# Performance work log

Hardware: AMD Instinct MI355X
Metric: run time of the kernel (lower is better)

The kernel has to match this reference:

```python
import jax, jax.numpy as jnp
import numpy as np

BSZ, SL, D, K, KU, KY, NPAD = 2, 1024, 768, 16, 3, 2, 2048


def setup_inputs() -> dict:
    key = jax.random.key(0)
    ks = jax.random.split(key, 8)
    s = 1.0 / np.sqrt(D).astype(np.float32)
    return {
        "inputs": jax.random.normal(ks[0], (BSZ, SL, D), dtype=jnp.float32),
        "sigma": jax.random.uniform(ks[1], (K,), dtype=jnp.float32, minval=1e-3, maxval=1.0),
        "V": jax.random.normal(ks[2], (SL, K), dtype=jnp.float32),
        "M_u": jax.random.normal(ks[3], (KU, D, D), dtype=jnp.float32) * s,
        "M_phi_plus": jax.random.normal(ks[4], (K, D, D), dtype=jnp.float32) * s,
        "M_phi_minus": jax.random.normal(ks[5], (K, D, D), dtype=jnp.float32) * s,
        "M_y": jax.random.normal(ks[6], (D, KY, D), dtype=jnp.float32) * s,
        "padded_sl": NPAD,
    }


def _shift(x, i):
    # prepend i zeros along the time axis, drop the last i steps
    if i == 0:
        return x
    return jnp.pad(x, ((0, 0), (i, 0), (0, 0)))[:, : x.shape[1]]


def _forward(inputs, sigma, V, M_u, M_phi_plus, M_phi_minus, M_y, padded_sl,
             use_ar_u=True, use_ar_y=True):
    bsz, sl, d = inputs.shape
    n = padded_sl
    sgn = jnp.where(jnp.arange(sl) % 2 == 0, 1.0, -1.0).astype(inputs.dtype)[None, :, None]
    # --- FFT long convolution of inputs against K spectral filters (compute_spectral) ---
    v_f = jnp.fft.rfft(V, n=n, axis=0)                           # (nf, K)
    u_k = jnp.stack([inputs, inputs * sgn], axis=-1)             # (b, sl, d, 2): plus / alternating-sign branches
    U_f = jnp.fft.rfft(u_k, n=n, axis=1)                         # (b, nf, d, 2)
    prod = v_f[None, :, :, None, None] * U_f[:, :, None, :, :]   # (b, nf, K, d, 2)
    U_conv = jnp.fft.irfft(prod, n=n, axis=1)[:, :sl]            # (b, sl, K, d, 2)
    U_plus = U_conv[..., 0]
    U_minus = U_conv[..., 1] * sgn[..., None]
    scale = sigma ** 0.25                                        # (K,) Hankel eigenvalue scaling
    spectral = (jnp.einsum('blkd,k,kdo->blo', U_plus, scale, M_phi_plus)
                + jnp.einsum('blkd,k,kdo->blo', U_minus, scale, M_phi_minus))
    if use_ar_y:
        spectral = _shift(spectral, 2)
    y_t = spectral
    if use_ar_u:
        # compute_ar_u: sum_i M_u[i] @ u_{t-i}
        ar_u = sum(jnp.einsum('bld,do->blo', _shift(inputs, i), M_u[i])
                   for i in range(M_u.shape[0]))
        y_t = y_t + ar_u
    if use_ar_y:
        # compute_ar_y: sum_{i=1..k_y} M_y[:, i-1, :] @ y_{t-i}
        ar_y = sum(jnp.einsum('bld,od->blo', _shift(y_t, i + 1), M_y[:, i, :])
                   for i in range(M_y.shape[1]))
        y_t = y_t + ar_y
    return y_t


def reference(inputs, sigma, V, M_u, M_phi_plus, M_phi_minus, M_y, padded_sl):
    # dropout rate is 0.0 -> identity at both dropout sites
    return _forward(inputs, sigma, V, M_u, M_phi_plus, M_phi_minus, M_y, padded_sl)
```

## Files before the change

### kernel.cpp

```cpp
#include <hip/hip_runtime.h>
#include <cstddef>
#include <cstdint>

#define SLEN 1024
#define DIM  768
#define NJ   32
#define KSPEC (NJ * DIM)
#define KTOT  (KSPEC + 3 * DIM)
#define MROWS (2 * SLEN)
#define SK1 8
#define SK2 4

typedef _Float16 f16;
typedef _Float16 f16x8 __attribute__((ext_vector_type(8)));
typedef _Float16 f16x4 __attribute__((ext_vector_type(4)));
typedef float    f32x4 __attribute__((ext_vector_type(4)));

__device__ __forceinline__ void async16(f16* lds, const f16* g) {
    __builtin_amdgcn_global_load_lds(
        (const __attribute__((address_space(1))) unsigned int*)g,
        (__attribute__((address_space(3))) unsigned int*)lds, 16, 0, 0);
}

__global__ __launch_bounds__(256) void build_r8(
    const float* __restrict__ sigma, const float* __restrict__ V,
    f16* __restrict__ R8, float* __restrict__ zb)
{
    int g = blockIdx.x * 256 + threadIdx.x;
    if (g < 256) zb[g] = 0.f;
    int j = g / 1536, i = g % 1536;
    int k = j & 15;
    int tau = 1031 - i;
    float val = 0.f;
    if (tau >= 0 && tau < 1024) {
        val = powf(sigma[k], 0.25f) * V[tau * 16 + k];
        if (j >= 16 && (tau & 1)) val = -val;
    }
    R8[j * 1536 + i] = (f16)val;
}

__global__ __launch_bounds__(256) void pack_x(
    const float* __restrict__ x, f16* __restrict__ x16, f16* __restrict__ x16t)
{
    __shared__ float tile[32][33];
    const int b  = blockIdx.z;
    const int d0 = blockIdx.y * 32;
    const int t0 = blockIdx.x * 32;
    const int tx = threadIdx.x & 31, ty = threadIdx.x >> 5;
#pragma unroll
    for (int r = 0; r < 4; ++r) {
        int tl = ty + r * 8;
        float v = x[(size_t)(b * SLEN + t0 + tl) * DIM + d0 + tx];
        tile[tl][tx] = v;
        x16[(size_t)(b * SLEN + t0 + tl) * DIM + d0 + tx] = (f16)v;
    }
    __syncthreads();
#pragma unroll
    for (int r = 0; r < 4; ++r) {
        int dl = ty + r * 8;
        x16t[((size_t)b * DIM + d0 + dl) * SLEN + t0 + tx] = (f16)tile[tx][dl];
    }
}

__global__ __launch_bounds__(256) void pack_w(
    const float* __restrict__ Mpp, const float* __restrict__ Mpm,
    const float* __restrict__ Mu, f16* __restrict__ W16t)
{
    __shared__ float tile[32][33];
    const int c0 = blockIdx.x * 32;
    const int o0 = blockIdx.y * 32;
    const int tx = threadIdx.x & 31, ty = threadIdx.x >> 5;
#pragma unroll
    for (int r = 0; r < 4; ++r) {
        int cl = ty + r * 8;
        int c = c0 + cl;
        const float* src;
        if (c < 12288)      src = Mpp + (size_t)c * DIM;
        else if (c < KSPEC) src = Mpm + (size_t)(c - 12288) * DIM;
        else                src = Mu  + (size_t)(c - KSPEC) * DIM;
        tile[cl][tx] = src[o0 + tx];
    }
    __syncthreads();
#pragma unroll
    for (int r = 0; r < 4; ++r) {
        int ol = ty + r * 8;
        W16t[(size_t)(o0 + ol) * KTOT + c0 + tx] = (f16)tile[tx][ol];
    }
}

__global__ __launch_bounds__(256) void pack_my(
    const float* __restrict__ My, f16* __restrict__ My16t)
{
    int g = blockIdx.x * 256 + threadIdx.x;
    float4 v = ((const float4*)My)[g];
    f16x4 h = {(f16)v.x, (f16)v.y, (f16)v.z, (f16)v.w};
    ((f16x4*)My16t)[g] = h;
}

__global__ __launch_bounds__(256) void conv_mfma(
    const f16* __restrict__ xt, const f16* __restrict__ R8,
    f16* __restrict__ U16)
{
    __shared__ f16 Bs[128 * 64];
    __shared__ f16 Cp[8 * 264];
    const int d0 = blockIdx.x * 128;
    const int l0 = blockIdx.y * 128;
    const int b  = blockIdx.z >> 5;
    const int j  = blockIdx.z & 31;
    const int tid = threadIdx.x;
    const int lane = tid & 63, w = tid >> 6;
    const int wr = w >> 1, wc = w & 1;
    const int lrow = lane & 15, lgrp = lane >> 4;
    const int rrel = lane >> 3, slotw = lane & 7;
    const int colh = (slotw ^ rrel) * 8;

    f32x4 acc[4][4];
#pragma unroll
    for (int mi = 0; mi < 4; ++mi)
#pragma unroll
        for (int ni = 0; ni < 4; ++ni) acc[mi][ni] = (f32x4){0.f, 0.f, 0.f, 0.f};

    const f16* R8j = R8 + j * 1536;
    const f16* xb  = xt + ((size_t)b * DIM + d0) * SLEN;
    const int cch = tid / 33;
    const int cjc = (tid % 33) * 8;
    const int nkt = (l0 >> 6) + 2;

    for (int kt = 0; kt < nkt; ++kt) {
        const int t0 = kt * 64;
        const int base = 904 - l0 + t0;
        {
            const f16* gp = R8j + base + cjc - cch;
            f16x8 v;
#pragma unroll
            for (int e = 0; e < 8; ++e) v[e] = gp[e];
            *(f16x8*)&Cp[cch * 264 + cjc] = v;
            if (tid < 8) {
                int ch2 = tid + 256;
                int c2 = ch2 / 33, jc2 = (ch2 % 33) * 8;
                const f16* gp2 = R8j + base + jc2 - c2;
                f16x8 v2;
#pragma unroll
                for (int e = 0; e < 8; ++e) v2[e] = gp2[e];
                *(f16x8*)&Cp[c2 * 264 + jc2] = v2;
            }
        }
#pragma unroll
        for (int q = 0; q < 4; ++q) {
            int row = w * 32 + q * 8 + rrel;
            async16(&Bs[(w * 32 + q * 8) * 64],
                    xb + (size_t)row * SLEN + t0 + colh);
        }
        __syncthreads();
#pragma unroll
        for (int ks = 0; ks < 2; ++ks) {
            f16x8 af[4], bf[4];
#pragma unroll
            for (int mi = 0; mi < 4; ++mi) {
                int r = wr * 64 + mi * 16 + lrow;
                int h = 127 - r + ks * 32 + lgrp * 8;
                int c = (-h) & 7;
                af[mi] = *(const f16x8*)&Cp[c * 265 + h];
            }
#pragma unroll
            for (int ni = 0; ni < 4; ++ni) {
                int col = wc * 64 + ni * 16 + lrow;
                int slot = (ks * 4 + lgrp) ^ (col & 7);
                bf[ni] = *(const f16x8*)&Bs[col * 64 + slot * 8];
            }
#pragma unroll
            for (int mi = 0; mi < 4; ++mi)
#pragma unroll
                for (int ni = 0; ni < 4; ++ni)
                    acc[mi][ni] = __builtin_amdgcn_mfma_f32_16x16x32_f16(
                        af[mi], bf[ni], acc[mi][ni], 0, 0, 0);
        }
        __syncthreads();
    }
    const size_t ub = (size_t)b * SLEN * KSPEC + (size_t)j * DIM;
#pragma unroll
    for (int mi = 0; mi < 4; ++mi)
#pragma unroll
        for (int ni = 0; ni < 4; ++ni) {
            int l = l0 + wr * 64 + mi * 16 + lgrp * 4;
            int d = d0 + wc * 64 + ni * 16 + lrow;
#pragma unroll
            for (int q = 0; q < 4; ++q)
                U16[ub + (size_t)(l + q) * KSPEC + d] = (f16)acc[mi][ni][q];
        }
}

__global__ __launch_bounds__(256) void gemm1_mfma(
    const f16* __restrict__ U16, const f16* __restrict__ x16,
    const f16* __restrict__ W16t, const f16* __restrict__ zb16,
    float* __restrict__ P)
{
    __shared__ f16 As[128 * 64];
    __shared__ f16 Bs[128 * 64];
    const int n0 = blockIdx.x * 128;
    const int m0 = blockIdx.y * 128;
    const int s  = blockIdx.z;
    const int tid = threadIdx.x;
    const int lane = tid & 63, w = tid >> 6;
    const int wr = w >> 1, wc = w & 1;
    const int lrow = lane & 15, lgrp = lane >> 4;
    const int rrel = lane >> 3, slotw = lane & 7;
    const int colh = (slotw ^ rrel) * 8;

    f32x4 acc[4][4];
#pragma unroll
    for (int mi = 0; mi < 4; ++mi)
#pragma unroll
        for (int ni = 0; ni < 4; ++ni) acc[mi][ni] = (f32x4){0.f, 0.f, 0.f, 0.f};

    const int kts = (420 * s) >> 3, kte = (420 * (s + 1)) >> 3;
    for (int kt = kts; kt < kte; ++kt) {
        const int c0 = kt * 64;
#pragma unroll
        for (int q = 0; q < 4; ++q) {
            int row = w * 32 + q * 8 + rrel;
            int m = m0 + row;
            int l = m & (SLEN - 1);
            const f16* src;
            if (c0 < KSPEC) {
                src = (l >= 2) ? U16 + (size_t)(m - 2) * KSPEC + c0 + colh : zb16;
            } else {
                int cr = c0 - KSPEC;
                int i  = cr / DIM;
                src = (l >= i) ? x16 + (size_t)(m - i) * DIM + (cr - i * DIM) + colh
                               : zb16;
            }
            async16(&As[(w * 32 + q * 8) * 64], src);
        }
#pragma unroll
        for (int q = 0; q < 4; ++q) {
            int row = w * 32 + q * 8 + rrel;
            async16(&Bs[(w * 32 + q * 8) * 64],
                    W16t + (size_t)(n0 + row) * KTOT + c0 + colh);
        }
        __syncthreads();
#pragma unroll
        for (int ks = 0; ks < 2; ++ks) {
            f16x8 af[4], bf[4];
#pragma unroll
            for (int mi = 0; mi < 4; ++mi) {
                int r = wr * 64 + mi * 16 + lrow;
                int slot = (ks * 4 + lgrp) ^ (r & 7);
                af[mi] = *(const f16x8*)&As[r * 64 + slot * 8];
            }
#pragma unroll
            for (int ni = 0; ni < 4; ++ni) {
                int col = wc * 64 + ni * 16 + lrow;
                int slot = (ks * 4 + lgrp) ^ (col & 7);
                bf[ni] = *(const f16x8*)&Bs[col * 64 + slot * 8];
            }
#pragma unroll
            for (int mi = 0; mi < 4; ++mi)
#pragma unroll
                for (int ni = 0; ni < 4; ++ni)
                    acc[mi][ni] = __builtin_amdgcn_mfma_f32_16x16x32_f16(
                        af[mi], bf[ni], acc[mi][ni], 0, 0, 0);
        }
        __syncthreads();
    }
    float* Pp = P + (size_t)s * MROWS * DIM;
#pragma unroll
    for (int mi = 0; mi < 4; ++mi)
#pragma unroll
        for (int ni = 0; ni < 4; ++ni) {
            int m = m0 + wr * 64 + mi * 16 + lgrp * 4;
            int col = n0 + wc * 64 + ni * 16 + lrow;
#pragma unroll
            for (int q = 0; q < 4; ++q)
                Pp[(size_t)(m + q) * DIM + col] = acc[mi][ni][q];
        }
}

__global__ __launch_bounds__(256) void reduce8(
    const float* __restrict__ P, float* __restrict__ z, f16* __restrict__ z16)
{
    int g = blockIdx.x * 256 + threadIdx.x;
    const float4* P4 = (const float4*)P;
    float4 s = P4[g];
#pragma unroll
    for (int i = 1; i < SK1; ++i) {
        float4 t = P4[g + (size_t)i * 393216];
        s.x += t.x; s.y += t.y; s.z += t.z; s.w += t.w;
    }
    ((float4*)z)[g] = s;
    f16x4 h = {(f16)s.x, (f16)s.y, (f16)s.z, (f16)s.w};
    ((f16x4*)z16)[g] = h;
}

__global__ __launch_bounds__(256) void gemm2_mfma(
    const f16* __restrict__ z16, const f16* __restrict__ My16t,
    const f16* __restrict__ zb16, float* __restrict__ P2)
{
    __shared__ f16 As[128 * 64];
    __shared__ f16 Bs[128 * 64];
    const int n0 = blockIdx.x * 128;
    const int m0 = blockIdx.y * 128;
    const int s  = blockIdx.z;
    const int tid = threadIdx.x;
    const int lane = tid & 63, w = tid >> 6;
    const int wr = w >> 1, wc = w & 1;
    const int lrow = lane & 15, lgrp = lane >> 4;
    const int rrel = lane >> 3, slotw = lane & 7;
    const int colh = (slotw ^ rrel) * 8;

    f32x4 acc[4][4];
#pragma unroll
    for (int mi = 0; mi < 4; ++mi)
#pragma unroll
        for (int ni = 0; ni < 4; ++ni) acc[mi][ni] = (f32x4){0.f, 0.f, 0.f, 0.f};

    for (int kt = s * 6; kt < (s + 1) * 6; ++kt) {
        const int c0 = kt * 64;
        const int i = (c0 >= DIM) ? 1 : 0;
        const int sh = i + 1;
        const int co = c0 - i * DIM;
#pragma unroll
        for (int q = 0; q < 4; ++q) {
            int row = w * 32 + q * 8 + rrel;
            int m = m0 + row;
            int l = m & (SLEN - 1);
            const f16* src = (l >= sh)
                ? z16 + (size_t)(m - sh) * DIM + co + colh : zb16;
            async16(&As[(w * 32 + q * 8) * 64], src);
        }
#pragma unroll
        for (int q = 0; q < 4; ++q) {
            int row = w * 32 + q * 8 + rrel;
            async16(&Bs[(w * 32 + q * 8) * 64],
                    My16t + (size_t)(n0 + row) * 1536 + c0 + colh);
        }
        __syncthreads();
#pragma unroll
        for (int ks = 0; ks < 2; ++ks) {
            f16x8 af[4], bf[4];
#pragma unroll
            for (int mi = 0; mi < 4; ++mi) {
                int r = wr * 64 + mi * 16 + lrow;
                int slot = (ks * 4 + lgrp) ^ (r & 7);
                af[mi] = *(const f16x8*)&As[r * 64 + slot * 8];
            }
#pragma unroll
            for (int ni = 0; ni < 4; ++ni) {
                int col = wc * 64 + ni * 16 + lrow;
                int slot = (ks * 4 + lgrp) ^ (col & 7);
                bf[ni] = *(const f16x8*)&Bs[col * 64 + slot * 8];
            }
#pragma unroll
            for (int mi = 0; mi < 4; ++mi)
#pragma unroll
                for (int ni = 0; ni < 4; ++ni)
                    acc[mi][ni] = __builtin_amdgcn_mfma_f32_16x16x32_f16(
                        af[mi], bf[ni], acc[mi][ni], 0, 0, 0);
        }
        __syncthreads();
    }
    float* Pp = P2 + (size_t)s * MROWS * DIM;
#pragma unroll
    for (int mi = 0; mi < 4; ++mi)
#pragma unroll
        for (int ni = 0; ni < 4; ++ni) {
            int m = m0 + wr * 64 + mi * 16 + lgrp * 4;
            int col = n0 + wc * 64 + ni * 16 + lrow;
#pragma unroll
            for (int q = 0; q < 4; ++q)
                Pp[(size_t)(m + q) * DIM + col] = acc[mi][ni][q];
        }
}

__global__ __launch_bounds__(256) void final_add(
    const float* __restrict__ z, const float* __restrict__ P2,
    float* __restrict__ out)
{
    int g = blockIdx.x * 256 + threadIdx.x;
    const float4* z4 = (const float4*)z;
    const float4* Q  = (const float4*)P2;
    float4 s = z4[g];
#pragma unroll
    for (int i = 0; i < SK2; ++i) {
        float4 t = Q[g + (size_t)i * 393216];
        s.x += t.x; s.y += t.y; s.z += t.z; s.w += t.w;
    }
    ((float4*)out)[g] = s;
}

extern "C" void kernel_launch(void* const* d_in, const int* in_sizes, int n_in,
                              void* d_out, int out_size, void* d_ws, size_t ws_size,
                              hipStream_t stream)
{
    const float* inputs = (const float*)d_in[0];
    const float* sigma  = (const float*)d_in[1];
    const float* V      = (const float*)d_in[2];
    const float* Mu     = (const float*)d_in[3];
    const float* Mpp    = (const float*)d_in[4];
    const float* Mpm    = (const float*)d_in[5];
    const float* My     = (const float*)d_in[6];
    float* out = (float*)d_out;

    char* base = (char*)d_ws;
    float* zb   = (float*)(base);
    f16* R8     = (f16*)(base + 1024);
    f16* x16    = (f16*)(base + 99328);
    f16* x16t   = (f16*)(base + 3245056);
    f16* W16t   = (f16*)(base + 6390784);
    f16* My16t  = (f16*)(base + 47678464);
    f16* U16    = (f16*)(base + 50037760);
    f16* z16    = (f16*)(base + 150701056);
    float* P    = (float*)(base + 153846784);
    float* z    = (float*)(base + 204178432);
    const f16* zb16 = (const f16*)zb;

    build_r8<<<192, 256, 0, stream>>>(sigma, V, R8, zb);
    pack_x<<<dim3(32, 24, 2), 256, 0, stream>>>(inputs, x16, x16t);
    pack_w<<<dim3(840, 24), 256, 0, stream>>>(Mpp, Mpm, Mu, W16t);
    pack_my<<<1152, 256, 0, stream>>>(My, My16t);
    conv_mfma<<<dim3(6, 8, 64), 256, 0, stream>>>(x16t, R8, U16);
    gemm1_mfma<<<dim3(6, 16, SK1), 256, 0, stream>>>(U16, x16, W16t, zb16, P);
    reduce8<<<1536, 256, 0, stream>>>(P, z, z16);
    gemm2_mfma<<<dim3(6, 16, SK2), 256, 0, stream>>>(z16, My16t, zb16, P);
    final_add<<<1536, 256, 0, stream>>>(z, P, out);
}
```

Baseline: 390.7 us.

## Reorder spectral path: project inputs by filter weights first, then convolve in time

The code now applies the M_phi projection (with the sigma^0.25 scale folded into the weights) to the inputs first, through one large GEMM. It then runs the Toeplitz time convolution on the projected outputs and accumulates over filters inside conv_b. Before, it convolved the inputs for all 32 filter branches and then ran a K=24576 GEMM. The AR-u term is split into its own GEMM and the split-K reduction is adjusted to match. The aim is to avoid writing and re-reading the large convolved intermediate and to lower the total FLOPs. In exchange, the intermediate Yt (32×768 by 2048 rows) must still be written and read, and the fp16 rounding happens at a different point.

Result: slower. 483.0 us (+23.6%).

```diff
diff --git a/kernel.cpp b/kernel.cpp
--- a/kernel.cpp
+++ b/kernel.cpp
@@ -5,11 +5,11 @@
 #define SLEN 1024
 #define DIM  768
 #define NJ   32
-#define KSPEC (NJ * DIM)
-#define KTOT  (KSPEC + 3 * DIM)
+#define NSPEC (NJ * DIM)
 #define MROWS (2 * SLEN)
-#define SK1 8
-#define SK2 4
+#define NP    (MROWS * DIM)
+#define SKAR  2
+#define SK2   4
 
 typedef _Float16 f16;
 typedef _Float16 f16x8 __attribute__((ext_vector_type(8)));
@@ -23,8 +23,7 @@
 }
 
 __global__ __launch_bounds__(256) void build_r8(
-    const float* __restrict__ sigma, const float* __restrict__ V,
-    f16* __restrict__ R8, float* __restrict__ zb)
+    const float* __restrict__ V, f16* __restrict__ R8, float* __restrict__ zb)
 {
     int g = blockIdx.x * 256 + threadIdx.x;
     if (g < 256) zb[g] = 0.f;
@@ -33,58 +32,61 @@
     int tau = 1031 - i;
     float val = 0.f;
     if (tau >= 0 && tau < 1024) {
-        val = powf(sigma[k], 0.25f) * V[tau * 16 + k];
+        val = V[tau * 16 + k];
         if (j >= 16 && (tau & 1)) val = -val;
     }
     R8[j * 1536 + i] = (f16)val;
 }
 
-__global__ __launch_bounds__(256) void pack_x(
-    const float* __restrict__ x, f16* __restrict__ x16, f16* __restrict__ x16t)
+__global__ __launch_bounds__(256) void pack_x16(
+    const float* __restrict__ x, f16* __restrict__ x16)
+{
+    int g = blockIdx.x * 256 + threadIdx.x;
+    float4 v = ((const float4*)x)[g];
+    f16x4 h = {(f16)v.x, (f16)v.y, (f16)v.z, (f16)v.w};
+    ((f16x4*)x16)[g] = h;
+}
+
+__global__ __launch_bounds__(256) void pack_wA(
+    const float* __restrict__ Mpp, const float* __restrict__ Mpm,
+    const float* __restrict__ sigma, f16* __restrict__ WAt)
 {
     __shared__ float tile[32][33];
-    const int b  = blockIdx.z;
-    const int d0 = blockIdx.y * 32;
-    const int t0 = blockIdx.x * 32;
+    const int d0 = blockIdx.x * 32, o0 = blockIdx.y * 32, j = blockIdx.z;
+    const int k = j & 15;
+    const float* src = (j < 16 ? Mpp : Mpm) + (size_t)k * DIM * DIM;
+    const float sc = powf(sigma[k], 0.25f);
     const int tx = threadIdx.x & 31, ty = threadIdx.x >> 5;
-#pragma unroll
-    for (int r = 0; r < 4; ++r) {
-        int tl = ty + r * 8;
-        float v = x[(size_t)(b * SLEN + t0 + tl) * DIM + d0 + tx];
-        tile[tl][tx] = v;
-        x16[(size_t)(b * SLEN + t0 + tl) * DIM + d0 + tx] = (f16)v;
-    }
-    __syncthreads();
 #pragma unroll
     for (int r = 0; r < 4; ++r) {
         int dl = ty + r * 8;
-        x16t[((size_t)b * DIM + d0 + dl) * SLEN + t0 + tx] = (f16)tile[tx][dl];
-    }
-}
-
-__global__ __launch_bounds__(256) void pack_w(
-    const float* __restrict__ Mpp, const float* __restrict__ Mpm,
-    const float* __restrict__ Mu, f16* __restrict__ W16t)
-{
-    __shared__ float tile[32][33];
-    const int c0 = blockIdx.x * 32;
-    const int o0 = blockIdx.y * 32;
-    const int tx = threadIdx.x & 31, ty = threadIdx.x >> 5;
-#pragma unroll
-    for (int r = 0; r < 4; ++r) {
-        int cl = ty + r * 8;
-        int c = c0 + cl;
-        const float* src;
-        if (c < 12288)      src = Mpp + (size_t)c * DIM;
-        else if (c < KSPEC) src = Mpm + (size_t)(c - 12288) * DIM;
-        else                src = Mu  + (size_t)(c - KSPEC) * DIM;
-        tile[cl][tx] = src[o0 + tx];
+        tile[dl][tx] = src[(size_t)(d0 + dl) * DIM + o0 + tx];
     }
     __syncthreads();
 #pragma unroll
     for (int r = 0; r < 4; ++r) {
         int ol = ty + r * 8;
-        W16t[(size_t)(o0 + ol) * KTOT + c0 + tx] = (f16)tile[tx][ol];
+        WAt[(size_t)(j * DIM + o0 + ol) * DIM + d0 + tx] = (f16)(sc * tile[tx][ol]);
+    }
+}
+
+__global__ __launch_bounds__(256) void pack_mu(
+    const float* __restrict__ Mu, f16* __restrict__ Mut)
+{
+    __shared__ float tile[32][33];
+    const int d0 = blockIdx.x * 32, o0 = blockIdx.y * 32, i = blockIdx.z;
+    const float* src = Mu + (size_t)i * DIM * DIM;
+    const int tx = threadIdx.x & 31, ty = threadIdx.x >> 5;
+#pragma unroll
+    for (int r = 0; r < 4; ++r) {
+        int dl = ty + r * 8;
+        tile[dl][tx] = src[(size_t)(d0 + dl) * DIM + o0 + tx];
+    }
+    __syncthreads();
+#pragma unroll
+    for (int r = 0; r < 4; ++r) {
+        int ol = ty + r * 8;
+        Mut[(size_t)(o0 + ol) * 2304 + i * DIM + d0 + tx] = (f16)tile[tx][ol];
     }
 }
 
@@ -97,16 +99,15 @@
     ((f16x4*)My16t)[g] = h;
 }
 
-__global__ __launch_bounds__(256) void conv_mfma(
-    const f16* __restrict__ xt, const f16* __restrict__ R8,
-    f16* __restrict__ U16)
-{
-    __shared__ f16 Bs[128 * 64];
-    __shared__ f16 Cp[8 * 264];
-    const int d0 = blockIdx.x * 128;
-    const int l0 = blockIdx.y * 128;
-    const int b  = blockIdx.z >> 5;
-    const int j  = blockIdx.z & 31;
+__global__ __launch_bounds__(256) void gemmA(
+    const f16* __restrict__ x16, const f16* __restrict__ WAt,
+    f16* __restrict__ Yt)
+{
+    __shared__ f16 smem[128 * 132];
+    f16* As = smem;
+    f16* Bs = smem + 8192;
+    const int n0 = blockIdx.x * 128;
+    const int m0 = blockIdx.y * 128;
     const int tid = threadIdx.x;
     const int lane = tid & 63, w = tid >> 6;
     const int wr = w >> 1, wc = w & 1;
@@ -120,36 +121,16 @@
 #pragma unroll
         for (int ni = 0; ni < 4; ++ni) acc[mi][ni] = (f32x4){0.f, 0.f, 0.f, 0.f};
 
-    const f16* R8j = R8 + j * 1536;
-    const f16* xb  = xt + ((size_t)b * DIM + d0) * SLEN;
-    const int cch = tid / 33;
-    const int cjc = (tid % 33) * 8;
-    const int nkt = (l0 >> 6) + 2;
-
-    for (int kt = 0; kt < nkt; ++kt) {
-        const int t0 = kt * 64;
-        const int base = 904 - l0 + t0;
-        {
-            const f16* gp = R8j + base + cjc - cch;
-            f16x8 v;
-#pragma unroll
-            for (int e = 0; e < 8; ++e) v[e] = gp[e];
-            *(f16x8*)&Cp[cch * 264 + cjc] = v;
-            if (tid < 8) {
-                int ch2 = tid + 256;
-                int c2 = ch2 / 33, jc2 = (ch2 % 33) * 8;
-                const f16* gp2 = R8j + base + jc2 - c2;
-                f16x8 v2;
-#pragma unroll
-                for (int e = 0; e < 8; ++e) v2[e] = gp2[e];
-                *(f16x8*)&Cp[c2 * 264 + jc2] = v2;
-            }
-        }
+#pragma unroll 1
+    for (int kt = 0; kt < 12; ++kt) {
+        const int c0 = kt * 64;
 #pragma unroll
         for (int q = 0; q < 4; ++q) {
             int row = w * 32 + q * 8 + rrel;
+            async16(&As[(w * 32 + q * 8) * 64],
+                    x16 + (size_t)(m0 + row) * DIM + c0 + colh);
             async16(&Bs[(w * 32 + q * 8) * 64],
-                    xb + (size_t)row * SLEN + t0 + colh);
+                    WAt + (size_t)(n0 + row) * DIM + c0 + colh);
         }
         __syncthreads();
 #pragma unroll
@@ -158,9 +139,8 @@
 #pragma unroll
             for (int mi = 0; mi < 4; ++mi) {
                 int r = wr * 64 + mi * 16 + lrow;
-                int h = 127 - r + ks * 32 + lgrp * 8;
-                int c = (-h) & 7;
-                af[mi] = *(const f16x8*)&Cp[c * 265 + h];
+                int slot = (ks * 4 + lgrp) ^ (r & 7);
+                af[mi] = *(const f16x8*)&As[r * 64 + slot * 8];
             }
 #pragma unroll
             for (int ni = 0; ni < 4; ++ni) {
@@ -177,23 +157,127 @@
         }
         __syncthreads();
     }
-    const size_t ub = (size_t)b * SLEN * KSPEC + (size_t)j * DIM;
 #pragma unroll
     for (int mi = 0; mi < 4; ++mi)
 #pragma unroll
         for (int ni = 0; ni < 4; ++ni) {
-            int l = l0 + wr * 64 + mi * 16 + lgrp * 4;
-            int d = d0 + wc * 64 + ni * 16 + lrow;
+            int col = wc * 64 + ni * 16 + lrow;
+            int rowm = wr * 64 + mi * 16 + lgrp * 4;
+            f16x4 hv = {(f16)acc[mi][ni][0], (f16)acc[mi][ni][1],
+                        (f16)acc[mi][ni][2], (f16)acc[mi][ni][3]};
+            *(f16x4*)&smem[col * 132 + rowm] = hv;
+        }
+    __syncthreads();
+    {
+        int row = tid >> 1, half = tid & 1;
+        const f16* cr = &smem[row * 132 + half * 64];
+        f16* gp = Yt + (size_t)(n0 + row) * MROWS + m0 + half * 64;
+#pragma unroll
+        for (int e = 0; e < 16; ++e)
+            *(f16x4*)&gp[e * 4] = *(const f16x4*)&cr[e * 4];
+    }
+}
+
+__global__ __launch_bounds__(256) void conv_b(
+    const f16* __restrict__ Yt, const f16* __restrict__ R8,
+    float* __restrict__ P)
+{
+    __shared__ f16 Bs[128 * 64];
+    __shared__ f16 Cp[8 * 264];
+    const int o0 = blockIdx.x * 128;
+    const int meff = blockIdx.y ^ 7;
+    const int b = meff >> 3, yp = meff & 7;
+    const int l0 = yp * 128, m0 = meff * 128;
+    const int jg = blockIdx.z;
+    const int tid = threadIdx.x;
+    const int lane = tid & 63, w = tid >> 6;
+    const int wr = w >> 1, wc = w & 1;
+    const int lrow = lane & 15, lgrp = lane >> 4;
+    const int rrel = lane >> 3, slotw = lane & 7;
+    const int colh = (slotw ^ rrel) * 8;
+    const int cch = tid / 33, cjc = (tid % 33) * 8;
+
+    f32x4 acc[4][4];
+#pragma unroll
+    for (int mi = 0; mi < 4; ++mi)
+#pragma unroll
+        for (int ni = 0; ni < 4; ++ni) acc[mi][ni] = (f32x4){0.f, 0.f, 0.f, 0.f};
+
+    const int nkt = yp * 2 + 2;
+#pragma unroll 1
+    for (int jj = 0; jj < 8; ++jj) {
+        const int j = jg * 8 + jj;
+        const f16* R8j = R8 + j * 1536;
+        const f16* Yb = Yt + ((size_t)(j * DIM + o0)) * MROWS + b * SLEN;
+#pragma unroll 1
+        for (int tt = 0; tt < nkt; ++tt) {
+            const int t0 = tt * 64;
+            const int cpb = 906 - (l0 - t0);
+            {
+                const f16* gp = R8j + cpb + cjc - cch;
+                f16x8 v;
+#pragma unroll
+                for (int e = 0; e < 8; ++e) v[e] = gp[e];
+                *(f16x8*)&Cp[cch * 264 + cjc] = v;
+                if (tid < 8) {
+                    int ch2 = tid + 256;
+                    int c2 = ch2 / 33, jc2 = (ch2 % 33) * 8;
+                    const f16* gp2 = R8j + cpb + jc2 - c2;
+                    f16x8 v2;
+#pragma unroll
+                    for (int e = 0; e < 8; ++e) v2[e] = gp2[e];
+                    *(f16x8*)&Cp[c2 * 264 + jc2] = v2;
+                }
+            }
+#pragma unroll
+            for (int q = 0; q < 4; ++q) {
+                int row = w * 32 + q * 8 + rrel;
+                async16(&Bs[(w * 32 + q * 8) * 64],
+                        Yb + (size_t)row * MROWS + t0 + colh);
+            }
+            __syncthreads();
+#pragma unroll
+            for (int ks = 0; ks < 2; ++ks) {
+                f16x8 af[4], bf[4];
+#pragma unroll
+                for (int mi = 0; mi < 4; ++mi) {
+                    int r = wr * 64 + mi * 16 + lrow;
+                    int h = 127 - r + ks * 32 + lgrp * 8;
+                    int c = (-h) & 7;
+                    af[mi] = *(const f16x8*)&Cp[c * 265 + h];
+                }
+#pragma unroll
+                for (int ni = 0; ni < 4; ++ni) {
+                    int col = wc * 64 + ni * 16 + lrow;
+                    int slot = (ks * 4 + lgrp) ^ (col & 7);
+                    bf[ni] = *(const f16x8*)&Bs[col * 64 + slot * 8];
+                }
+#pragma unroll
+                for (int mi = 0; mi < 4; ++mi)
+#pragma unroll
+                    for (int ni = 0; ni < 4; ++ni)
+                        acc[mi][ni] = __builtin_amdgcn_mfma_f32_16x16x32_f16(
+                            af[mi], bf[ni], acc[mi][ni], 0, 0, 0);
+            }
+            __syncthreads();
+        }
+    }
+    float* Pp = P + (size_t)jg * NP;
+#pragma unroll
+    for (int mi = 0; mi < 4; ++mi)
+#pragma unroll
+        for (int ni = 0; ni < 4; ++ni) {
+            int m = m0 + wr * 64 + mi * 16 + lgrp * 4;
+            int col = o0 + wc * 64 + ni * 16 + lrow;
 #pragma unroll
             for (int q = 0; q < 4; ++q)
-                U16[ub + (size_t)(l + q) * KSPEC + d] = (f16)acc[mi][ni][q];
-        }
-}
-
-__global__ __launch_bounds__(256) void gemm1_mfma(
-    const f16* __restrict__ U16, const f16* __restrict__ x16,
-    const f16* __restrict__ W16t, const f16* __restrict__ zb16,
-    float* __restrict__ P)
+                Pp[(size_t)(m + q) * DIM + col] = acc[mi][ni][q];
+        }
+}
+
+__global__ __launch_bounds__(256) void ar_gemm(
+    const f16* __restrict__ x16, const f16* __restrict__ Mut,
+    const f16* __restrict__ zb16, float* __restrict__ P)
 {
     __shared__ f16 As[128 * 64];
     __shared__ f16 Bs[128 * 64];
@@ -213,30 +297,24 @@
 #pragma unroll
         for (int ni = 0; ni < 4; ++ni) acc[mi][ni] = (f32x4){0.f, 0.f, 0.f, 0.f};
 
-    const int kts = (420 * s) >> 3, kte = (420 * (s + 1)) >> 3;
-    for (int kt = kts; kt < kte; ++kt) {
+    for (int kt = s * 18; kt < (s + 1) * 18; ++kt) {
         const int c0 = kt * 64;
+        const int i = c0 / DIM;
+        const int co = c0 - i * DIM;
 #pragma unroll
         for (int q = 0; q < 4; ++q) {
             int row = w * 32 + q * 8 + rrel;
             int m = m0 + row;
             int l = m & (SLEN - 1);
-            const f16* src;
-            if (c0 < KSPEC) {
-                src = (l >= 2) ? U16 + (size_t)(m - 2) * KSPEC + c0 + colh : zb16;
-            } else {
-                int cr = c0 - KSPEC;
-                int i  = cr / DIM;
-                src = (l >= i) ? x16 + (size_t)(m - i) * DIM + (cr - i * DIM) + colh
-                               : zb16;
-            }
+            const f16* src = (l >= i)
+                ? x16 + (size_t)(m - i) * DIM + co + colh : zb16;
             async16(&As[(w * 32 + q * 8) * 64], src);
         }
 #pragma unroll
         for (int q = 0; q < 4; ++q) {
             int row = w * 32 + q * 8 + rrel;
             async16(&Bs[(w * 32 + q * 8) * 64],
-                    W16t + (size_t)(n0 + row) * KTOT + c0 + colh);
+                    Mut + (size_t)(n0 + row) * 2304 + c0 + colh);
         }
         __syncthreads();
 #pragma unroll
@@ -263,7 +341,7 @@
         }
         __syncthreads();
     }
-    float* Pp = P + (size_t)s * MROWS * DIM;
+    float* Pp = P + (size_t)(4 + s) * NP;
 #pragma unroll
     for (int mi = 0; mi < 4; ++mi)
 #pragma unroll
@@ -276,15 +354,15 @@
         }
 }
 
-__global__ __launch_bounds__(256) void reduce8(
+__global__ __launch_bounds__(256) void zreduce(
     const float* __restrict__ P, float* __restrict__ z, f16* __restrict__ z16)
 {
     int g = blockIdx.x * 256 + threadIdx.x;
     const float4* P4 = (const float4*)P;
     float4 s = P4[g];
 #pragma unroll
-    for (int i = 1; i < SK1; ++i) {
-        float4 t = P4[g + (size_t)i * 393216];
+    for (int i = 1; i < 6; ++i) {
+        float4 t = P4[g + (size_t)i * (NP / 4)];
         s.x += t.x; s.y += t.y; s.z += t.z; s.w += t.w;
     }
     ((float4*)z)[g] = s;
@@ -359,7 +437,7 @@
         }
         __syncthreads();
     }
-    float* Pp = P2 + (size_t)s * MROWS * DIM;
+    float* Pp = P2 + (size_t)s * NP;
 #pragma unroll
     for (int mi = 0; mi < 4; ++mi)
 #pragma unroll
@@ -382,7 +460,7 @@
     float4 s = z4[g];
 #pragma unroll
     for (int i = 0; i < SK2; ++i) {
-        float4 t = Q[g + (size_t)i * 393216];
+        float4 t = Q[g + (size_t)i * (NP / 4)];
         s.x += t.x; s.y += t.y; s.z += t.z; s.w += t.w;
     }
     ((float4*)out)[g] = s;
@@ -405,22 +483,24 @@
     float* zb   = (float*)(base);
     f16* R8     = (f16*)(base + 1024);
     f16* x16    = (f16*)(base + 99328);
-    f16* x16t   = (f16*)(base + 3245056);
-    f16* W16t   = (f16*)(base + 6390784);
-    f16* My16t  = (f16*)(base + 47678464);
-    f16* U16    = (f16*)(base + 50037760);
-    f16* z16    = (f16*)(base + 150701056);
-    float* P    = (float*)(base + 153846784);
-    float* z    = (float*)(base + 204178432);
+    f16* WAt    = (f16*)(base + 3245056);
+    f16* Mut    = (f16*)(base + 40993792);
+    f16* My16t  = (f16*)(base + 44532736);
+    f16* Yt     = (f16*)(base + 46892032);
+    float* P    = (float*)(base + 147555328);
+    float* z    = (float*)(base + 185304064);
+    f16* z16    = (f16*)(base + 191595520);
     const f16* zb16 = (const f16*)zb;
 
-    build_r8<<<192, 256, 0, stream>>>(sigma, V, R8, zb);
-    pack_x<<<dim3(32, 24, 2), 256, 0, stream>>>(inputs, x16, x16t);
-    pack_w<<<dim3(840, 24), 256, 0, stream>>>(Mpp, Mpm, Mu, W16t);
+    build_r8<<<192, 256, 0, stream>>>(V, R8, zb);
+    pack_x16<<<1536, 256, 0, stream>>>(inputs, x16);
+    pack_wA<<<dim3(24, 24, 32), 256, 0, stream>>>(Mpp, Mpm, sigma, WAt);
+    pack_mu<<<dim3(24, 24, 3), 256, 0, stream>>>(Mu, Mut);
     pack_my<<<1152, 256, 0, stream>>>(My, My16t);
-    conv_mfma<<<dim3(6, 8, 64), 256, 0, stream>>>(x16t, R8, U16);
-    gemm1_mfma<<<dim3(6, 16, SK1), 256, 0, stream>>>(U16, x16, W16t, zb16, P);
-    reduce8<<<1536, 256, 0, stream>>>(P, z, z16);
+    gemmA<<<dim3(192, 16), 256, 0, stream>>>(x16, WAt, Yt);
+    conv_b<<<dim3(6, 16, 4), 256, 0, stream>>>(Yt, R8, P);
+    ar_gemm<<<dim3(6, 16, SKAR), 256, 0, stream>>>(x16, Mut, zb16, P);
+    zreduce<<<1536, 256, 0, stream>>>(P, z, z16);
     gemm2_mfma<<<dim3(6, 16, SK2), 256, 0, stream>>>(z16, My16t, zb16, P);
     final_add<<<1536, 256, 0, stream>>>(z, P, out);
 }
```
